# Kernel tuning notes

Measured on AMD Instinct MI355X. Metric: run time of the kernel, lower is better.

The kernel has to match this reference:

```python
import jax, jax.numpy as jnp
import numpy as np

OUT_H, OUT_W = 64, 64  # glimpse size (layer's output_dim)
B, IMG_H, IMG_W, CH = 32, 512, 512, 3


def setup_inputs() -> dict:
    key = jax.random.key(0)
    k_img, k_u, k_s, k_d, k_u2, k_s2, k_d2 = jax.random.split(key, 7)
    img_tensor = jax.random.uniform(k_img, (B, IMG_H, IMG_W, CH), dtype=jnp.float32)
    # DRAW-style params per sample: (uy, sy, dy, ux, sx, dx)
    # centres u in [0, img - glimpse], sigma s in [1, 5], stride d in [1, img/glimpse]
    uy = jax.random.uniform(k_u, (B, 1), minval=0.0, maxval=IMG_H - OUT_H * 2.0)
    sy = jax.random.uniform(k_s, (B, 1), minval=1.0, maxval=5.0)
    dy = jax.random.uniform(k_d, (B, 1), minval=1.0, maxval=IMG_H / OUT_H)
    ux = jax.random.uniform(k_u2, (B, 1), minval=0.0, maxval=IMG_W - OUT_W * 2.0)
    sx = jax.random.uniform(k_s2, (B, 1), minval=1.0, maxval=5.0)
    dx = jax.random.uniform(k_d2, (B, 1), minval=1.0, maxval=IMG_W / OUT_W)
    transform_params = jnp.concatenate([uy, sy, dy, ux, sx, dx], axis=-1)  # (B, 6)
    return {"img_tensor": img_tensor, "transform_params": transform_params}


def gaussian_mask(u, s, d, R, C):
    """Normalized Gaussian filterbank.
    u, s, d: (B, 1) centre of first Gaussian, std, stride between centres.
    R: number of glimpse rows/cols; C: image size along that axis.
    Returns (B, C, R), each column normalized to sum 1 (plus eps)."""
    r = jnp.arange(R, dtype=jnp.float32).reshape(1, 1, R)
    c = jnp.arange(C, dtype=jnp.float32).reshape(1, C, 1)
    centres = u[:, None, :] + r * d[:, None, :]            # (B, 1, R)
    mask = jnp.exp(-0.5 * jnp.square((c - centres) / s[:, None, :]))  # (B, C, R)
    return mask / (jnp.sum(mask, axis=1, keepdims=True) + 1e-8)


def reference(img_tensor, transform_params):
    # img_tensor: (B, h, w, ch); transform_params: (B, 6)
    _, h, w, _ = img_tensor.shape
    uy, sy, dy, ux, sx, dx = jnp.split(transform_params, 6, axis=-1)
    Ay = gaussian_mask(uy, sy, dy, OUT_H, h)  # (B, h, OUT_H)
    Ax = gaussian_mask(ux, sx, dx, OUT_W, w)  # (B, w, OUT_W)
    # glimpse = Ay^T @ img @ Ax, applied per channel
    g = jnp.einsum('bhH,bhwc->bHwc', Ay, img_tensor)   # (B, OUT_H, w, ch)
    return jnp.einsum('bHwc,bwW->bHWc', g, Ax)         # (B, OUT_H, OUT_W, ch)
```

## Files before the change

kernel.cpp:

```cpp
#include <hip/hip_runtime.h>

#define BATCH 32
#define IMG 512
#define CH 3
#define GOUT 64
#define ROWB (IMG*CH)

typedef __attribute__((ext_vector_type(8))) short  short8;
typedef __attribute__((ext_vector_type(4))) float  floatx4;

__device__ __forceinline__ unsigned short f2bf(float x) {
    unsigned u = __builtin_bit_cast(unsigned, x);
    u += 0x7FFFu + ((u >> 16) & 1u);
    return (unsigned short)(u >> 16);
}

__global__ __launch_bounds__(64) void mask_kernel(const float* __restrict__ tp,
                                                  unsigned short* __restrict__ AyT,
                                                  unsigned short* __restrict__ AxT) {
    int blk  = blockIdx.x;
    int r    = blk & 63;
    int axis = (blk >> 6) & 1;
    int b    = blk >> 7;

    const float* p = tp + b*6 + (axis ? 3 : 0);
    float u = p[0], s = p[1], d = p[2];
    float centre = u + (float)r * d;
    float inv_s  = 1.0f / s;

    int lane = threadIdx.x;
    float e[8];
    float sum = 0.0f;
    #pragma unroll
    for (int i = 0; i < 8; ++i) {
        float z = ((float)(i*64 + lane) - centre) * inv_s;
        e[i] = __expf(-0.5f * z * z);
        sum += e[i];
    }
    #pragma unroll
    for (int m = 1; m < 64; m <<= 1)
        sum += __shfl_xor(sum, m, 64);
    float inv_sum = 1.0f / (sum + 1e-8f);

    unsigned short* dst = (axis ? AxT : AyT) + ((size_t)b*GOUT + r) * IMG;
    #pragma unroll
    for (int i = 0; i < 8; ++i)
        dst[i*64 + lane] = f2bf(e[i] * inv_sum);
}

__global__ __launch_bounds__(256) void stage1_kernel(const float* __restrict__ img,
                                                     const unsigned short* __restrict__ AyT,
                                                     float* __restrict__ gP) {
    int tile = blockIdx.x % 24;
    int b    = blockIdx.x / 24;
    int tid  = threadIdx.x;
    int wave = tid >> 6;
    int lane = tid & 63;
    int n16  = lane & 15;
    int q    = lane >> 4;
    int wc   = tile*64 + wave*16 + n16;

    floatx4 acc[4];
    #pragma unroll
    for (int mt = 0; mt < 4; ++mt) acc[mt] = (floatx4){0.f, 0.f, 0.f, 0.f};

    const unsigned short* ayb = AyT + ((size_t)b*GOUT + n16) * IMG;

    for (int h0 = 0; h0 < IMG; h0 += 32) {
        const float* bp = img + ((size_t)(b*IMG + h0 + q*8)) * ROWB + wc;
        short8 bf;
        #pragma unroll
        for (int j = 0; j < 8; ++j)
            bf[j] = (short)f2bf(bp[(size_t)j * ROWB]);

        #pragma unroll
        for (int mt = 0; mt < 4; ++mt) {
            short8 af = *(const short8*)(ayb + (size_t)mt*16*IMG + h0 + q*8);
            acc[mt] = __builtin_amdgcn_mfma_f32_16x16x32_bf16(af, bf, acc[mt], 0, 0, 0);
        }
    }

    int c = wc % 3, w = wc / 3;
    float* gb = gP + ((size_t)(b*CH + c) * GOUT) * IMG + w;
    #pragma unroll
    for (int mt = 0; mt < 4; ++mt) {
        int Hbase = mt*16 + q*4;
        #pragma unroll
        for (int reg = 0; reg < 4; ++reg)
            gb[(size_t)(Hbase + reg) * IMG] = acc[mt][reg];
    }
}

__global__ __launch_bounds__(256) void stage2_kernel(const float* __restrict__ gP,
                                                     const unsigned short* __restrict__ AxT,
                                                     float* __restrict__ out) {
    int blk  = blockIdx.x;
    int part = blk & 3;
    int bc   = blk >> 2;
    int c    = bc % 3;
    int b    = bc / 3;
    int tid  = threadIdx.x;
    int wm   = tid >> 6;
    int lane = tid & 63;
    int n16  = lane & 15;
    int q    = lane >> 4;

    floatx4 acc[4];
    #pragma unroll
    for (int nt = 0; nt < 4; ++nt) acc[nt] = (floatx4){0.f, 0.f, 0.f, 0.f};

    const float*          ga  = gP  + ((size_t)(b*CH + c) * GOUT + wm*16 + n16) * IMG;
    const unsigned short* axb = AxT + ((size_t)b*GOUT + n16) * IMG;

    #pragma unroll
    for (int cc = 0; cc < 4; ++cc) {
        int w0 = part*128 + cc*32;
        const float* ap = ga + w0 + q*8;
        short8 af;
        #pragma unroll
        for (int j = 0; j < 8; ++j)
            af[j] = (short)f2bf(ap[j]);

        #pragma unroll
        for (int nt = 0; nt < 4; ++nt) {
            short8 bf = *(const short8*)(axb + (size_t)nt*16*IMG + w0 + q*8);
            acc[nt] = __builtin_amdgcn_mfma_f32_16x16x32_bf16(af, bf, acc[nt], 0, 0, 0);
        }
    }

    #pragma unroll
    for (int nt = 0; nt < 4; ++nt) {
        int W = nt*16 + n16;
        #pragma unroll
        for (int reg = 0; reg < 4; ++reg) {
            int H = wm*16 + q*4 + reg;
            atomicAdd(out + (((size_t)b*GOUT + H) * GOUT + W) * CH + c, acc[nt][reg]);
        }
    }
}

extern "C" void kernel_launch(void* const* d_in, const int* in_sizes, int n_in,
                              void* d_out, int out_size, void* d_ws, size_t ws_size,
                              hipStream_t stream) {
    const float* img = (const float*)d_in[0];
    const float* tp  = (const float*)d_in[1];
    float* out = (float*)d_out;

    unsigned short* AyT = (unsigned short*)d_ws;
    unsigned short* AxT = AyT + (size_t)BATCH * GOUT * IMG;
    float*          gP  = (float*)(AxT + (size_t)BATCH * GOUT * IMG);

    hipMemsetAsync(d_out, 0, (size_t)out_size * sizeof(float), stream);
    mask_kernel  <<<BATCH * 2 * GOUT,  64, 0, stream>>>(tp, AyT, AxT);
    stage1_kernel<<<BATCH * 24,       256, 0, stream>>>(img, AyT, gP);
    stage2_kernel<<<BATCH * CH * 4,   256, 0, stream>>>(gP, AxT, out);
}
```

Baseline: 190.1 us.

## Replace stage1 MFMA with scalar FMA over split-K row partitions in bf16

Stage 1 now uses scalar fp32 FMAs instead of bf16 MFMA. Each thread owns one image column and computes all 64 glimpse rows over a 128-row slice of the image, reading Ay as wave-uniform broadcast loads from a transposed fp32 mask. Split-K partial results go out as bf16 in four planes, and stage 2 sums those planes while loading. The aim is fully coalesced single reads of the image and smaller intermediates, at the cost of 64 FMAs per loaded element and extra bf16 rounding of the partial sums.

```diff
diff --git a/kernel.cpp b/kernel.cpp
--- a/kernel.cpp
+++ b/kernel.cpp
@@ -1,10 +1,12 @@
 #include <hip/hip_runtime.h>
+#include <stdint.h>
 
 #define BATCH 32
 #define IMG 512
 #define CH 3
 #define GOUT 64
 #define ROWB (IMG*CH)
+#define GPLANE ((size_t)BATCH*CH*GOUT*IMG)
 
 typedef __attribute__((ext_vector_type(8))) short  short8;
 typedef __attribute__((ext_vector_type(4))) float  floatx4;
@@ -14,9 +16,12 @@
     u += 0x7FFFu + ((u >> 16) & 1u);
     return (unsigned short)(u >> 16);
 }
+__device__ __forceinline__ float b2f(short s) {
+    return __builtin_bit_cast(float, ((unsigned)(unsigned short)s) << 16);
+}
 
 __global__ __launch_bounds__(64) void mask_kernel(const float* __restrict__ tp,
-                                                  unsigned short* __restrict__ AyT,
+                                                  float* __restrict__ AyF,
                                                   unsigned short* __restrict__ AxT) {
     int blk  = blockIdx.x;
     int r    = blk & 63;
@@ -42,56 +47,60 @@
         sum += __shfl_xor(sum, m, 64);
     float inv_sum = 1.0f / (sum + 1e-8f);
 
-    unsigned short* dst = (axis ? AxT : AyT) + ((size_t)b*GOUT + r) * IMG;
-    #pragma unroll
-    for (int i = 0; i < 8; ++i)
-        dst[i*64 + lane] = f2bf(e[i] * inv_sum);
+    if (axis) {
+        unsigned short* dst = AxT + ((size_t)b*GOUT + r) * IMG;
+        #pragma unroll
+        for (int i = 0; i < 8; ++i)
+            dst[i*64 + lane] = f2bf(e[i] * inv_sum);
+    } else {
+        #pragma unroll
+        for (int i = 0; i < 8; ++i)
+            AyF[((size_t)b*IMG + i*64 + lane) * GOUT + r] = e[i] * inv_sum;
+    }
 }
 
 __global__ __launch_bounds__(256) void stage1_kernel(const float* __restrict__ img,
-                                                     const unsigned short* __restrict__ AyT,
-                                                     float* __restrict__ gP) {
-    int tile = blockIdx.x % 24;
-    int b    = blockIdx.x / 24;
-    int tid  = threadIdx.x;
-    int wave = tid >> 6;
-    int lane = tid & 63;
-    int n16  = lane & 15;
-    int q    = lane >> 4;
-    int wc   = tile*64 + wave*16 + n16;
+                                                     const float* __restrict__ Ay,
+                                                     unsigned short* __restrict__ gB) {
+    int blk  = blockIdx.x;
+    int part = blk & 3;
+    int bj   = blk >> 2;
+    int jc   = bj % 6;
+    int b    = bj / 6;
+    int wc   = jc*256 + threadIdx.x;
+    int w    = wc / 3;
+    int c    = wc - 3*w;
 
-    floatx4 acc[4];
+    const float* imgp = img + ((size_t)b*IMG + part*128) * ROWB + wc;
+    const float* ayp  = Ay  + ((size_t)b*IMG + part*128) * GOUT;
+
+    floatx4 acc[16];
     #pragma unroll
-    for (int mt = 0; mt < 4; ++mt) acc[mt] = (floatx4){0.f, 0.f, 0.f, 0.f};
+    for (int k = 0; k < 16; ++k) acc[k] = (floatx4){0.f, 0.f, 0.f, 0.f};
 
-    const unsigned short* ayb = AyT + ((size_t)b*GOUT + n16) * IMG;
-
-    for (int h0 = 0; h0 < IMG; h0 += 32) {
-        const float* bp = img + ((size_t)(b*IMG + h0 + q*8)) * ROWB + wc;
-        short8 bf;
+    #pragma unroll 4
+    for (int h = 0; h < 128; ++h) {
+        float v = imgp[(size_t)h * ROWB];
+        const float* ar = ayp + (size_t)h * GOUT;
         #pragma unroll
-        for (int j = 0; j < 8; ++j)
-            bf[j] = (short)f2bf(bp[(size_t)j * ROWB]);
-
-        #pragma unroll
-        for (int mt = 0; mt < 4; ++mt) {
-            short8 af = *(const short8*)(ayb + (size_t)mt*16*IMG + h0 + q*8);
-            acc[mt] = __builtin_amdgcn_mfma_f32_16x16x32_bf16(af, bf, acc[mt], 0, 0, 0);
+        for (int k = 0; k < 16; ++k) {
+            acc[k][0] = fmaf(ar[k*4+0], v, acc[k][0]);
+            acc[k][1] = fmaf(ar[k*4+1], v, acc[k][1]);
+            acc[k][2] = fmaf(ar[k*4+2], v, acc[k][2]);
+            acc[k][3] = fmaf(ar[k*4+3], v, acc[k][3]);
         }
     }
 
-    int c = wc % 3, w = wc / 3;
-    float* gb = gP + ((size_t)(b*CH + c) * GOUT) * IMG + w;
+    unsigned short* gp = gB + (size_t)part*GPLANE
+                       + ((size_t)(b*CH + c) * GOUT) * IMG + w;
     #pragma unroll
-    for (int mt = 0; mt < 4; ++mt) {
-        int Hbase = mt*16 + q*4;
+    for (int k = 0; k < 16; ++k)
         #pragma unroll
-        for (int reg = 0; reg < 4; ++reg)
-            gb[(size_t)(Hbase + reg) * IMG] = acc[mt][reg];
-    }
+        for (int r = 0; r < 4; ++r)
+            gp[(size_t)(k*4 + r) * IMG] = f2bf(acc[k][r]);
 }
 
-__global__ __launch_bounds__(256) void stage2_kernel(const float* __restrict__ gP,
+__global__ __launch_bounds__(256) void stage2_kernel(const unsigned short* __restrict__ gB,
                                                      const unsigned short* __restrict__ AxT,
                                                      float* __restrict__ out) {
     int blk  = blockIdx.x;
@@ -109,17 +118,20 @@
     #pragma unroll
     for (int nt = 0; nt < 4; ++nt) acc[nt] = (floatx4){0.f, 0.f, 0.f, 0.f};
 
-    const float*          ga  = gP  + ((size_t)(b*CH + c) * GOUT + wm*16 + n16) * IMG;
+    const unsigned short* ga  = gB  + ((size_t)(b*CH + c) * GOUT + wm*16 + n16) * IMG;
     const unsigned short* axb = AxT + ((size_t)b*GOUT + n16) * IMG;
 
     #pragma unroll
     for (int cc = 0; cc < 4; ++cc) {
         int w0 = part*128 + cc*32;
-        const float* ap = ga + w0 + q*8;
+        short8 s0 = *(const short8*)(ga + w0 + q*8);
+        short8 s1 = *(const short8*)(ga + GPLANE   + w0 + q*8);
+        short8 s2 = *(const short8*)(ga + 2*GPLANE + w0 + q*8);
+        short8 s3 = *(const short8*)(ga + 3*GPLANE + w0 + q*8);
         short8 af;
         #pragma unroll
         for (int j = 0; j < 8; ++j)
-            af[j] = (short)f2bf(ap[j]);
+            af[j] = (short)f2bf((b2f(s0[j]) + b2f(s1[j])) + (b2f(s2[j]) + b2f(s3[j])));
 
         #pragma unroll
         for (int nt = 0; nt < 4; ++nt) {
@@ -146,12 +158,12 @@
     const float* tp  = (const float*)d_in[1];
     float* out = (float*)d_out;
 
-    unsigned short* AyT = (unsigned short*)d_ws;
-    unsigned short* AxT = AyT + (size_t)BATCH * GOUT * IMG;
-    float*          gP  = (float*)(AxT + (size_t)BATCH * GOUT * IMG);
+    float*          AyF = (float*)d_ws;
+    unsigned short* AxT = (unsigned short*)(AyF + (size_t)BATCH * IMG * GOUT);
+    unsigned short* gB  = AxT + (size_t)BATCH * GOUT * IMG;
 
     hipMemsetAsync(d_out, 0, (size_t)out_size * sizeof(float), stream);
-    mask_kernel  <<<BATCH * 2 * GOUT,  64, 0, stream>>>(tp, AyT, AxT);
-    stage1_kernel<<<BATCH * 24,       256, 0, stream>>>(img, AyT, gP);
-    stage2_kernel<<<BATCH * CH * 4,   256, 0, stream>>>(gP, AxT, out);
+    mask_kernel  <<<BATCH * 2 * GOUT,  64, 0, stream>>>(tp, AyF, AxT);
+    stage1_kernel<<<BATCH * 6 * 4,    256, 0, stream>>>(img, AyF, gB);
+    stage2_kernel<<<BATCH * CH * 4,   256, 0, stream>>>(gB, AxT, out);
 }
```

After: 226.9 us. +19.4%, slower.
